# Performance work log

Hardware: AMD Instinct MI355X
Metric: run time of the kernel (lower is better)

## Reference

```python
import jax, jax.numpy as jnp
import numpy as np

jax.config.update("jax_enable_x64", True)

N = 100000   # active sparse sites
H = W = 512  # event-camera grid
CIN, CMID, COUT = 64, 384, 64
SHIFT = 16   # shift_n


def setup_inputs() -> dict:
    rng = np.random.default_rng(0)
    # unique active coordinates on the grid (batch index 0)
    flat = rng.permutation(H * W)[:N]
    ys, xs = flat // W, flat % W
    # dense index map with 1-pixel halo; sentinel N = missing neighbor
    idx_map = np.full((H + 2, W + 2), N, dtype=np.int32)
    idx_map[ys + 1, xs + 1] = np.arange(N, dtype=np.int32)
    # 3x3 neighborhood indices per active site, row-major kernel order
    nbr = np.stack([idx_map[ys + 1 + dy, xs + 1 + dx]
                    for dy in (-1, 0, 1) for dx in (-1, 0, 1)], axis=1)

    def ri(lo, hi, shape):
        return jnp.asarray(rng.integers(lo, hi, size=shape), dtype=jnp.float32)

    return {
        "feats": ri(-128, 128, (N, CIN)),      # int8-valued input features
        "w1": ri(-128, 128, (CIN, CMID)),       # 1x1 expand weights
        "b1": ri(-1024, 1024, (CMID,)),
        "s1": ri(1, 16, (CMID,)),
        "w_dw": ri(-128, 128, (9, CMID)),       # 3x3 depthwise weights [k, C]
        "b2": ri(-1024, 1024, (CMID,)),
        "s2": ri(1, 64, (CMID,)),
        "w3": ri(-128, 128, (CMID, COUT)),      # 1x1 project weights
        "b3": ri(-1024, 1024, (COUT,)),
        "s3": ri(1, 16, (COUT,)),
        "neighbor_idx": jnp.asarray(nbr),       # [N, 9] int32, N = sentinel
    }


def _quant(psum, bias, scale, relu):
    # (psum + bias) * scale, add 2^(shift-1), arithmetic >> shift,
    # clamp to int8 range, optional relu. psum values are exact integers.
    t = psum.astype(jnp.int64)
    t = ((t + bias.astype(jnp.int64)) * scale.astype(jnp.int64)
         + (1 << (SHIFT - 1))) >> SHIFT
    y = jnp.clip(t.astype(jnp.float32), -128.0, 127.0)
    return jnp.maximum(y, 0.0) if relu else y


def reference(feats, w1, b1, s1, w_dw, b2, s2, w3, b3, s3, neighbor_idx):
    # 1x1 expand (sparse 1x1 conv == matmul over active sites) + quant + relu
    x1 = _quant(feats @ w1, b1, s1, True)                       # [N, CMID]
    # 3x3 depthwise sparse conv: gather 9 neighbors (zero row for missing)
    pad = jnp.concatenate([x1, jnp.zeros((1, x1.shape[1]), x1.dtype)], axis=0)
    psum2 = jnp.einsum('nkc,kc->nc', pad[neighbor_idx], w_dw)   # [N, CMID]
    x2 = _quant(psum2, b2, s2, True)
    # 1x1 project + quant (linear bottleneck: no relu)
    x3 = _quant(x2 @ w3, b3, s3, False)                          # [N, COUT]
    return x3
```

## Files before the change

kernel.cpp:

```cpp
#include <hip/hip_runtime.h>
#include <stdint.h>

#define N_SITES 100000
#define NPAD    100032
#define CIN 64
#define CMID 384
#define COUT 64
#define SHIFT 16

typedef int   v4i __attribute__((ext_vector_type(4)));
typedef unsigned int v4u __attribute__((ext_vector_type(4)));
typedef float v4f __attribute__((ext_vector_type(4)));

__global__ __launch_bounds__(256) void pack_w(
    const float* __restrict__ w1, const float* __restrict__ w3,
    const float* __restrict__ b1, const float* __restrict__ s1,
    const float* __restrict__ b2, const float* __restrict__ s2,
    const float* __restrict__ b3, const float* __restrict__ s3,
    const float* __restrict__ wdw,
    int8_t* __restrict__ w1p, int8_t* __restrict__ w3p,
    int* __restrict__ q1, int* __restrict__ q3,
    int8_t* __restrict__ wdw8, int* __restrict__ bs2,
    int8_t* __restrict__ x1s)
{
    int o = blockIdx.x * 256 + threadIdx.x;
    if (o < 24 * 64 * 16) {
        int t = o >> 10, l = (o >> 4) & 63, b = o & 15;
        int k = ((l >> 4) << 4) + b;
        int col = t * 16 + (l & 15);
        w1p[o] = (int8_t)__float2int_rn(w1[k * CMID + col]);
    }
    int o3 = o - 24 * 64 * 16;
    if (o3 >= 0 && o3 < 6 * 4 * 64 * 16) {
        int ks = o3 >> 12, t = (o3 >> 10) & 3;
        int l = (o3 >> 4) & 63, b = o3 & 15;
        int k = ks * 64 + ((l >> 4) << 4) + b;
        int col = t * 16 + (l & 15);
        w3p[o3] = (int8_t)__float2int_rn(w3[k * COUT + col]);
    }
    if (o < 9 * CMID)
        wdw8[o] = (int8_t)__float2int_rn(wdw[o]);
    if (o < CMID) {
        q1[o] = __float2int_rn(b1[o]);
        q1[CMID + o] = __float2int_rn(s1[o]);
        int bb = __float2int_rn(b2[o]);
        int ss = __float2int_rn(s2[o]);
        bs2[o] = (bb & 0xFFFF) | (ss << 16);
        x1s[(size_t)N_SITES * CMID + o] = 0;
    }
    if (o < COUT) {
        q3[o] = __float2int_rn(b3[o]);
        q3[COUT + o] = __float2int_rn(s3[o]);
    }
}

__global__ __launch_bounds__(256) void k1_mfma(
    const float* __restrict__ feats, const int8_t* __restrict__ w1p,
    const int* __restrict__ q1, int8_t* __restrict__ x1s)
{
    __shared__ int8_t xt[64 * 400];
    const int lane = threadIdx.x & 63;
    const int wave = threadIdx.x >> 6;
    const int sl = wave * 16 + (lane & 15);
    const int site = blockIdx.x * 64 + sl;
    const int rsite = min(site, N_SITES - 1);
    const int cb = (lane >> 4) << 2;

    v4i b;
    const float* fp = feats + (size_t)rsite * CIN + ((lane >> 4) << 4);
#pragma unroll
    for (int j = 0; j < 4; ++j) {
        const v4f f = *(const v4f*)(fp + 4 * j);
        uint32_t pk = (uint32_t)(__float2int_rn(f[0]) & 255)
                    | ((uint32_t)(__float2int_rn(f[1]) & 255) << 8)
                    | ((uint32_t)(__float2int_rn(f[2]) & 255) << 16)
                    | ((uint32_t)__float2int_rn(f[3]) << 24);
        b[j] = (int)pk;
    }

    const v4i* ap = (const v4i*)w1p + lane;
#pragma unroll
    for (int t = 0; t < 24; ++t) {
        v4i a = ap[t * 64];
        v4i acc = {0, 0, 0, 0};
        acc = __builtin_amdgcn_mfma_i32_16x16x64_i8(a, b, acc, 0, 0, 0);
        const int co = t * 16 + cb;
        const v4i bi = *(const v4i*)(q1 + co);
        const v4i si = *(const v4i*)(q1 + CMID + co);
        uint32_t wrd = 0;
#pragma unroll
        for (int r = 0; r < 4; ++r) {
            int v = ((acc[r] + bi[r]) * si[r] + (1 << (SHIFT - 1))) >> SHIFT;
            v = max(0, min(127, v));
            wrd |= (uint32_t)v << (8 * r);
        }
        *(uint32_t*)(xt + sl * 400 + co) = wrd;
    }
    __syncthreads();

    int8_t* dst = x1s + (size_t)blockIdx.x * 64 * CMID;
#pragma unroll
    for (int it = 0; it < 6; ++it) {
        const int lin = it * 4096 + threadIdx.x * 16;
        const int r = lin / 384;
        const int c = lin - r * 384;
        const v4u val = *(const v4u*)(xt + r * 400 + c);
        if (blockIdx.x * 64 + r < N_SITES)
            *(v4u*)(dst + lin) = val;
    }
}

__global__ __launch_bounds__(256) void k2_dw(
    const int8_t* __restrict__ x1s, const int* __restrict__ nbr,
    const int8_t* __restrict__ wdw8, const int* __restrict__ bs2,
    int8_t* __restrict__ x2s)
{
    const int g = blockIdx.x * 256 + threadIdx.x;
    const int site = g / 24;
    const int c0 = (g - site * 24) << 4;

    const int* nb = &nbr[site * 9];
    int idx[9];
#pragma unroll
    for (int k = 0; k < 9; ++k) idx[k] = nb[k];

    v4u V[9];
#pragma unroll
    for (int k = 0; k < 9; ++k) {
        const int off = (idx[k] << 8) + (idx[k] << 7) + c0;
        V[k] = *(const v4u*)(x1s + off);
    }

    int acc[16];
#pragma unroll
    for (int j = 0; j < 16; ++j) acc[j] = 0;

#pragma unroll
    for (int k = 0; k < 9; ++k) {
        const v4u W = *(const v4u*)(wdw8 + k * CMID + c0);
#pragma unroll
        for (int j = 0; j < 4; ++j) {
#pragma unroll
            for (int b = 0; b < 4; ++b) {
                const int v = (int)(uint8_t)(V[k][j] >> (8 * b));
                const int w = (int)(int8_t)(W[j] >> (8 * b));
                acc[j * 4 + b] += v * w;
            }
        }
    }

    const v4i BS0 = *(const v4i*)(bs2 + c0);
    const v4i BS1 = *(const v4i*)(bs2 + c0 + 4);
    const v4i BS2 = *(const v4i*)(bs2 + c0 + 8);
    const v4i BS3 = *(const v4i*)(bs2 + c0 + 12);
    const v4i BS[4] = {BS0, BS1, BS2, BS3};

    v4u outw;
#pragma unroll
    for (int j = 0; j < 4; ++j) {
        uint32_t wrd = 0;
#pragma unroll
        for (int b = 0; b < 4; ++b) {
            const int bsv = BS[j][b];
            const int bb = (bsv << 16) >> 16;
            const int ss = bsv >> 16;
            int t = ((acc[j * 4 + b] + bb) * ss + (1 << (SHIFT - 1))) >> SHIFT;
            t = max(0, min(127, t));
            wrd |= (uint32_t)t << (8 * b);
        }
        outw[j] = wrd;
    }
    *(v4u*)(x2s + (site << 8) + (site << 7) + c0) = outw;
}

__global__ __launch_bounds__(256) void k3_mfma(
    const int8_t* __restrict__ x2s, const int8_t* __restrict__ w3p,
    const int* __restrict__ q3, float* __restrict__ out)
{
    __shared__ float ot[64 * 68];
    const int lane = threadIdx.x & 63;
    const int wave = threadIdx.x >> 6;
    const int sl = wave * 16 + (lane & 15);
    const int site = blockIdx.x * 64 + sl;
    const int rsite = min(site, N_SITES - 1);
    const int cb = (lane >> 4) << 2;
    const int8_t* xrow = x2s + (size_t)rsite * CMID + ((lane >> 4) << 4);

    v4i acc[4] = {{0,0,0,0},{0,0,0,0},{0,0,0,0},{0,0,0,0}};
#pragma unroll
    for (int ks = 0; ks < 6; ++ks) {
        const v4i bfr = *(const v4i*)(xrow + ks * 64);
#pragma unroll
        for (int t = 0; t < 4; ++t) {
            const v4i afr = *((const v4i*)w3p + (ks * 4 + t) * 64 + lane);
            acc[t] = __builtin_amdgcn_mfma_i32_16x16x64_i8(afr, bfr, acc[t], 0, 0, 0);
        }
    }
#pragma unroll
    for (int t = 0; t < 4; ++t) {
        const int co = t * 16 + cb;
        const v4i bo = *(const v4i*)(q3 + co);
        const v4i so = *(const v4i*)(q3 + COUT + co);
        v4f o;
#pragma unroll
        for (int r = 0; r < 4; ++r) {
            int v = ((acc[t][r] + bo[r]) * so[r] + (1 << (SHIFT - 1))) >> SHIFT;
            v = max(-128, min(127, v));
            o[r] = (float)v;
        }
        *(v4f*)(&ot[sl * 68 + co]) = o;
    }
    __syncthreads();

    float* dst = out + (size_t)blockIdx.x * 64 * COUT;
#pragma unroll
    for (int it = 0; it < 4; ++it) {
        const int lin = it * 1024 + threadIdx.x * 4;
        const int r = lin >> 6;
        const int c = lin & 63;
        const v4f val = *(const v4f*)(&ot[r * 68 + c]);
        if (blockIdx.x * 64 + r < N_SITES)
            *(v4f*)(dst + lin) = val;
    }
}

extern "C" void kernel_launch(void* const* d_in, const int* in_sizes, int n_in,
                              void* d_out, int out_size, void* d_ws, size_t ws_size,
                              hipStream_t stream) {
    const float* feats = (const float*)d_in[0];
    const float* w1    = (const float*)d_in[1];
    const float* b1    = (const float*)d_in[2];
    const float* s1    = (const float*)d_in[3];
    const float* wdw   = (const float*)d_in[4];
    const float* b2    = (const float*)d_in[5];
    const float* s2    = (const float*)d_in[6];
    const float* w3    = (const float*)d_in[7];
    const float* b3    = (const float*)d_in[8];
    const float* s3    = (const float*)d_in[9];
    const int*   nbr   = (const int*)d_in[10];
    float* out = (float*)d_out;

    int8_t* x1s   = (int8_t*)d_ws;
    int8_t* x2s   = x1s + (size_t)NPAD * CMID;
    int8_t* w1p   = x2s + (size_t)NPAD * CMID;
    int8_t* w3p   = w1p + 24 * 64 * 16;
    int*    q1    = (int*)(w3p + 6 * 4 * 64 * 16);
    int*    q3    = q1 + 2 * CMID;
    int8_t* wdw8  = (int8_t*)(q3 + 2 * COUT);
    int*    bs2   = (int*)(wdw8 + 9 * CMID);

    pack_w<<<192, 256, 0, stream>>>(w1, w3, b1, s1, b2, s2, b3, s3, wdw,
                                    w1p, w3p, q1, q3, wdw8, bs2, x1s);
    k1_mfma<<<NPAD / 64, 256, 0, stream>>>(feats, w1p, q1, x1s);
    k2_dw<<<N_SITES * 24 / 256, 256, 0, stream>>>(x1s, nbr, wdw8, bs2, x2s);
    k3_mfma<<<NPAD / 64, 256, 0, stream>>>(x2s, w3p, q3, out);
}
```

Before: 82.65 us.

## Fuse depthwise conv and projection matmul into one kernel via LDS staging

Merges the 3x3 depthwise gather kernel and the 1x1 projection MFMA kernel into a single 768-thread kernel handling 32 sites per block. The depthwise results are written to shared memory instead of a global x2 buffer, and two waves then run the MFMA projection from LDS. This removes the x2 global write and read round trip plus one launch. The cost is that 10 of 12 waves sit idle during the MFMA phase, and the large blocks may reduce occupancy.

```diff
diff --git a/kernel.cpp b/kernel.cpp
--- a/kernel.cpp
+++ b/kernel.cpp
@@ -110,117 +110,116 @@
     }
 }
 
-__global__ __launch_bounds__(256) void k2_dw(
+__global__ __launch_bounds__(768) void k23(
     const int8_t* __restrict__ x1s, const int* __restrict__ nbr,
     const int8_t* __restrict__ wdw8, const int* __restrict__ bs2,
-    int8_t* __restrict__ x2s)
+    const int8_t* __restrict__ w3p, const int* __restrict__ q3,
+    float* __restrict__ out)
 {
-    const int g = blockIdx.x * 256 + threadIdx.x;
-    const int site = g / 24;
-    const int c0 = (g - site * 24) << 4;
-
-    const int* nb = &nbr[site * 9];
-    int idx[9];
-#pragma unroll
-    for (int k = 0; k < 9; ++k) idx[k] = nb[k];
-
-    v4u V[9];
-#pragma unroll
-    for (int k = 0; k < 9; ++k) {
-        const int off = (idx[k] << 8) + (idx[k] << 7) + c0;
-        V[k] = *(const v4u*)(x1s + off);
-    }
-
-    int acc[16];
-#pragma unroll
-    for (int j = 0; j < 16; ++j) acc[j] = 0;
-
-#pragma unroll
-    for (int k = 0; k < 9; ++k) {
-        const v4u W = *(const v4u*)(wdw8 + k * CMID + c0);
+    __shared__ int8_t xt[32 * 400];
+    __shared__ float  ot[32 * 68];
+    const int tid = threadIdx.x;
+
+    {
+        const int sl = tid / 24;
+        const int c0 = (tid - sl * 24) << 4;
+        const int site = blockIdx.x * 32 + sl;
+
+        const int* nb = &nbr[site * 9];
+        int idx[9];
+#pragma unroll
+        for (int k = 0; k < 9; ++k) idx[k] = nb[k];
+
+        v4u V[9];
+#pragma unroll
+        for (int k = 0; k < 9; ++k) {
+            const int off = (idx[k] << 8) + (idx[k] << 7) + c0;
+            V[k] = *(const v4u*)(x1s + off);
+        }
+
+        int acc[16];
+#pragma unroll
+        for (int j = 0; j < 16; ++j) acc[j] = 0;
+
+#pragma unroll
+        for (int k = 0; k < 9; ++k) {
+            const v4u W = *(const v4u*)(wdw8 + k * CMID + c0);
+#pragma unroll
+            for (int j = 0; j < 4; ++j) {
+#pragma unroll
+                for (int b = 0; b < 4; ++b) {
+                    const int v = (int)(uint8_t)(V[k][j] >> (8 * b));
+                    const int w = (int)(int8_t)(W[j] >> (8 * b));
+                    acc[j * 4 + b] += v * w;
+                }
+            }
+        }
+
+        const v4i BS0 = *(const v4i*)(bs2 + c0);
+        const v4i BS1 = *(const v4i*)(bs2 + c0 + 4);
+        const v4i BS2 = *(const v4i*)(bs2 + c0 + 8);
+        const v4i BS3 = *(const v4i*)(bs2 + c0 + 12);
+        const v4i BS[4] = {BS0, BS1, BS2, BS3};
+
+        v4u outw;
 #pragma unroll
         for (int j = 0; j < 4; ++j) {
+            uint32_t wrd = 0;
 #pragma unroll
             for (int b = 0; b < 4; ++b) {
-                const int v = (int)(uint8_t)(V[k][j] >> (8 * b));
-                const int w = (int)(int8_t)(W[j] >> (8 * b));
-                acc[j * 4 + b] += v * w;
-            }
-        }
-    }
-
-    const v4i BS0 = *(const v4i*)(bs2 + c0);
-    const v4i BS1 = *(const v4i*)(bs2 + c0 + 4);
-    const v4i BS2 = *(const v4i*)(bs2 + c0 + 8);
-    const v4i BS3 = *(const v4i*)(bs2 + c0 + 12);
-    const v4i BS[4] = {BS0, BS1, BS2, BS3};
-
-    v4u outw;
-#pragma unroll
-    for (int j = 0; j < 4; ++j) {
-        uint32_t wrd = 0;
-#pragma unroll
-        for (int b = 0; b < 4; ++b) {
-            const int bsv = BS[j][b];
-            const int bb = (bsv << 16) >> 16;
-            const int ss = bsv >> 16;
-            int t = ((acc[j * 4 + b] + bb) * ss + (1 << (SHIFT - 1))) >> SHIFT;
-            t = max(0, min(127, t));
-            wrd |= (uint32_t)t << (8 * b);
-        }
-        outw[j] = wrd;
-    }
-    *(v4u*)(x2s + (site << 8) + (site << 7) + c0) = outw;
-}
-
-__global__ __launch_bounds__(256) void k3_mfma(
-    const int8_t* __restrict__ x2s, const int8_t* __restrict__ w3p,
-    const int* __restrict__ q3, float* __restrict__ out)
-{
-    __shared__ float ot[64 * 68];
-    const int lane = threadIdx.x & 63;
-    const int wave = threadIdx.x >> 6;
-    const int sl = wave * 16 + (lane & 15);
-    const int site = blockIdx.x * 64 + sl;
-    const int rsite = min(site, N_SITES - 1);
-    const int cb = (lane >> 4) << 2;
-    const int8_t* xrow = x2s + (size_t)rsite * CMID + ((lane >> 4) << 4);
-
-    v4i acc[4] = {{0,0,0,0},{0,0,0,0},{0,0,0,0},{0,0,0,0}};
-#pragma unroll
-    for (int ks = 0; ks < 6; ++ks) {
-        const v4i bfr = *(const v4i*)(xrow + ks * 64);
+                const int bsv = BS[j][b];
+                const int bb = (bsv << 16) >> 16;
+                const int ss = bsv >> 16;
+                int t = ((acc[j * 4 + b] + bb) * ss + (1 << (SHIFT - 1))) >> SHIFT;
+                t = max(0, min(127, t));
+                wrd |= (uint32_t)t << (8 * b);
+            }
+            outw[j] = wrd;
+        }
+        *(v4u*)(xt + sl * 400 + c0) = outw;
+    }
+    __syncthreads();
+
+    const int wv = tid >> 6;
+    if (wv < 2) {
+        const int lane = tid & 63;
+        const int sl2 = wv * 16 + (lane & 15);
+        const int cb = (lane >> 4) << 2;
+        const int8_t* xrow = xt + sl2 * 400 + ((lane >> 4) << 4);
+
+        v4i acc[4] = {{0,0,0,0},{0,0,0,0},{0,0,0,0},{0,0,0,0}};
+#pragma unroll
+        for (int ks = 0; ks < 6; ++ks) {
+            const v4i bfr = *(const v4i*)(xrow + ks * 64);
+#pragma unroll
+            for (int t = 0; t < 4; ++t) {
+                const v4i afr = *((const v4i*)w3p + (ks * 4 + t) * 64 + lane);
+                acc[t] = __builtin_amdgcn_mfma_i32_16x16x64_i8(afr, bfr, acc[t], 0, 0, 0);
+            }
+        }
 #pragma unroll
         for (int t = 0; t < 4; ++t) {
-            const v4i afr = *((const v4i*)w3p + (ks * 4 + t) * 64 + lane);
-            acc[t] = __builtin_amdgcn_mfma_i32_16x16x64_i8(afr, bfr, acc[t], 0, 0, 0);
-        }
-    }
-#pragma unroll
-    for (int t = 0; t < 4; ++t) {
-        const int co = t * 16 + cb;
-        const v4i bo = *(const v4i*)(q3 + co);
-        const v4i so = *(const v4i*)(q3 + COUT + co);
-        v4f o;
-#pragma unroll
-        for (int r = 0; r < 4; ++r) {
-            int v = ((acc[t][r] + bo[r]) * so[r] + (1 << (SHIFT - 1))) >> SHIFT;
-            v = max(-128, min(127, v));
-            o[r] = (float)v;
-        }
-        *(v4f*)(&ot[sl * 68 + co]) = o;
+            const int co = t * 16 + cb;
+            const v4i bo = *(const v4i*)(q3 + co);
+            const v4i so = *(const v4i*)(q3 + COUT + co);
+            v4f o;
+#pragma unroll
+            for (int r = 0; r < 4; ++r) {
+                int v = ((acc[t][r] + bo[r]) * so[r] + (1 << (SHIFT - 1))) >> SHIFT;
+                v = max(-128, min(127, v));
+                o[r] = (float)v;
+            }
+            *(v4f*)(&ot[sl2 * 68 + co]) = o;
+        }
     }
     __syncthreads();
 
-    float* dst = out + (size_t)blockIdx.x * 64 * COUT;
-#pragma unroll
-    for (int it = 0; it < 4; ++it) {
-        const int lin = it * 1024 + threadIdx.x * 4;
+    if (tid < 512) {
+        const int lin = tid * 4;
         const int r = lin >> 6;
         const int c = lin & 63;
         const v4f val = *(const v4f*)(&ot[r * 68 + c]);
-        if (blockIdx.x * 64 + r < N_SITES)
-            *(v4f*)(dst + lin) = val;
+        *(v4f*)(out + (size_t)blockIdx.x * 32 * COUT + lin) = val;
     }
 }
 
@@ -241,8 +240,7 @@
     float* out = (float*)d_out;
 
     int8_t* x1s   = (int8_t*)d_ws;
-    int8_t* x2s   = x1s + (size_t)NPAD * CMID;
-    int8_t* w1p   = x2s + (size_t)NPAD * CMID;
+    int8_t* w1p   = x1s + (size_t)(NPAD + 64) * CMID;
     int8_t* w3p   = w1p + 24 * 64 * 16;
     int*    q1    = (int*)(w3p + 6 * 4 * 64 * 16);
     int*    q3    = q1 + 2 * CMID;
@@ -252,6 +250,5 @@
     pack_w<<<192, 256, 0, stream>>>(w1, w3, b1, s1, b2, s2, b3, s3, wdw,
                                     w1p, w3p, q1, q3, wdw8, bs2, x1s);
     k1_mfma<<<NPAD / 64, 256, 0, stream>>>(feats, w1p, q1, x1s);
-    k2_dw<<<N_SITES * 24 / 256, 256, 0, stream>>>(x1s, nbr, wdw8, bs2, x2s);
-    k3_mfma<<<NPAD / 64, 256, 0, stream>>>(x2s, w3p, q3, out);
-}
+    k23<<<N_SITES / 32, 768, 0, stream>>>(x1s, nbr, wdw8, bs2, w3p, q3, out);
+}
```

New measurement: 91.01 us. +10.1%, slower.

## Compute depthwise 3x3 conv with i8 MFMA using diagonal-packed weights

Applied to the files above, without the earlier changes.

The scalar per-thread depthwise kernel is replaced by a kernel that treats each 16-channel group as an MFMA 16x16x64 i8 product. The weight matrix is packed so each 16-wide tap block is diagonal, which lets the gathered neighbor rows act as the B operand. Outputs are staged in LDS and written back as coalesced rows. The MFMA path does 16x redundant multiplies on zero weights and changes the gather pattern, aiming to offload the int multiply-accumulate work from the VALU.

```diff
diff --git a/kernel.cpp b/kernel.cpp
--- a/kernel.cpp
+++ b/kernel.cpp
@@ -19,8 +19,8 @@
     const float* __restrict__ b3, const float* __restrict__ s3,
     const float* __restrict__ wdw,
     int8_t* __restrict__ w1p, int8_t* __restrict__ w3p,
-    int* __restrict__ q1, int* __restrict__ q3,
-    int8_t* __restrict__ wdw8, int* __restrict__ bs2,
+    int8_t* __restrict__ w2t,
+    int* __restrict__ q1, int* __restrict__ q3, int* __restrict__ bs2,
     int8_t* __restrict__ x1s)
 {
     int o = blockIdx.x * 256 + threadIdx.x;
@@ -38,8 +38,20 @@
         int col = t * 16 + (l & 15);
         w3p[o3] = (int8_t)__float2int_rn(w3[k * COUT + col]);
     }
-    if (o < 9 * CMID)
-        wdw8[o] = (int8_t)__float2int_rn(wdw[o]);
+    int o4 = o - 48 * 64 * 16;
+    if (o4 >= 0 && o4 < 24 * 3 * 64 * 16) {
+        int cg = o4 / 3072;
+        int rem = o4 - cg * 3072;
+        int kk = rem >> 10;
+        int l  = (rem >> 4) & 63;
+        int b  = o4 & 15;
+        int q  = l >> 4;
+        int tap = kk * 4 + q;
+        int8_t val = 0;
+        if (tap < 9 && b == (l & 15))
+            val = (int8_t)__float2int_rn(wdw[tap * CMID + cg * 16 + b]);
+        w2t[o4] = val;
+    }
     if (o < CMID) {
         q1[o] = __float2int_rn(b1[o]);
         q1[CMID + o] = __float2int_rn(s1[o]);
@@ -110,67 +122,64 @@
     }
 }
 
-__global__ __launch_bounds__(256) void k2_dw(
+__global__ __launch_bounds__(128) void k2_mfma(
     const int8_t* __restrict__ x1s, const int* __restrict__ nbr,
-    const int8_t* __restrict__ wdw8, const int* __restrict__ bs2,
+    const int8_t* __restrict__ w2t, const int* __restrict__ bs2,
     int8_t* __restrict__ x2s)
 {
-    const int g = blockIdx.x * 256 + threadIdx.x;
-    const int site = g / 24;
-    const int c0 = (g - site * 24) << 4;
-
-    const int* nb = &nbr[site * 9];
-    int idx[9];
-#pragma unroll
-    for (int k = 0; k < 9; ++k) idx[k] = nb[k];
-
-    v4u V[9];
-#pragma unroll
-    for (int k = 0; k < 9; ++k) {
-        const int off = (idx[k] << 8) + (idx[k] << 7) + c0;
-        V[k] = *(const v4u*)(x1s + off);
-    }
-
-    int acc[16];
-#pragma unroll
-    for (int j = 0; j < 16; ++j) acc[j] = 0;
-
-#pragma unroll
-    for (int k = 0; k < 9; ++k) {
-        const v4u W = *(const v4u*)(wdw8 + k * CMID + c0);
-#pragma unroll
-        for (int j = 0; j < 4; ++j) {
-#pragma unroll
-            for (int b = 0; b < 4; ++b) {
-                const int v = (int)(uint8_t)(V[k][j] >> (8 * b));
-                const int w = (int)(int8_t)(W[j] >> (8 * b));
-                acc[j * 4 + b] += v * w;
-            }
-        }
-    }
-
-    const v4i BS0 = *(const v4i*)(bs2 + c0);
-    const v4i BS1 = *(const v4i*)(bs2 + c0 + 4);
-    const v4i BS2 = *(const v4i*)(bs2 + c0 + 8);
-    const v4i BS3 = *(const v4i*)(bs2 + c0 + 12);
-    const v4i BS[4] = {BS0, BS1, BS2, BS3};
-
-    v4u outw;
-#pragma unroll
-    for (int j = 0; j < 4; ++j) {
+    __shared__ int8_t xt[2][16 * 400];
+    const int lane = threadIdx.x & 63;
+    const int wv = threadIdx.x >> 6;
+    const int site0 = (blockIdx.x * 2 + wv) * 16;
+    int8_t* xw = &xt[wv][0];
+    const int q  = lane >> 4;
+    const int sl = lane & 15;
+    const int site = site0 + sl;
+
+    int off[3];
+#pragma unroll
+    for (int kk = 0; kk < 3; ++kk) {
+        int tap = kk * 4 + q;
+        if (tap > 8) tap = 8;
+        const int idx = nbr[site * 9 + tap];
+        off[kk] = (idx << 8) + (idx << 7);
+    }
+
+#pragma unroll 1
+    for (int cg = 0; cg < 24; ++cg) {
+        const int c0 = cg << 4;
+        v4i acc = {0, 0, 0, 0};
+#pragma unroll
+        for (int kk = 0; kk < 3; ++kk) {
+            const v4i bfr = *(const v4i*)(x1s + off[kk] + c0);
+            const v4i afr = *((const v4i*)w2t + (cg * 3 + kk) * 64 + lane);
+            acc = __builtin_amdgcn_mfma_i32_16x16x64_i8(afr, bfr, acc, 0, 0, 0);
+        }
+        const v4i bsv = *(const v4i*)(bs2 + c0 + (q << 2));
         uint32_t wrd = 0;
 #pragma unroll
-        for (int b = 0; b < 4; ++b) {
-            const int bsv = BS[j][b];
-            const int bb = (bsv << 16) >> 16;
-            const int ss = bsv >> 16;
-            int t = ((acc[j * 4 + b] + bb) * ss + (1 << (SHIFT - 1))) >> SHIFT;
+        for (int r = 0; r < 4; ++r) {
+            const int bb = (bsv[r] << 16) >> 16;
+            const int ss = bsv[r] >> 16;
+            int t = ((acc[r] + bb) * ss + (1 << (SHIFT - 1))) >> SHIFT;
             t = max(0, min(127, t));
-            wrd |= (uint32_t)t << (8 * b);
-        }
-        outw[j] = wrd;
-    }
-    *(v4u*)(x2s + (site << 8) + (site << 7) + c0) = outw;
+            wrd |= (uint32_t)t << (8 * r);
+        }
+        *(uint32_t*)(xw + sl * 400 + c0 + (q << 2)) = wrd;
+    }
+
+    __builtin_amdgcn_wave_barrier();
+    asm volatile("s_waitcnt lgkmcnt(0)" ::: "memory");
+    __builtin_amdgcn_wave_barrier();
+
+    int8_t* dst = x2s + (size_t)site0 * CMID;
+#pragma unroll
+    for (int it = 0; it < 6; ++it) {
+        const int lin = it * 1024 + lane * 16;
+        const int r = lin / 384;
+        const int c = lin - r * 384;
+        *(v4u*)(dst + lin) = *(const v4u*)(xw + r * 400 + c);
+    }
 }
 
 __global__ __launch_bounds__(256) void k3_mfma(
@@ -240,18 +249,18 @@
     const int*   nbr   = (const int*)d_in[10];
     float* out = (float*)d_out;
 
-    int8_t* x1s   = (int8_t*)d_ws;
-    int8_t* x2s   = x1s + (size_t)NPAD * CMID;
-    int8_t* w1p   = x2s + (size_t)NPAD * CMID;
-    int8_t* w3p   = w1p + 24 * 64 * 16;
-    int*    q1    = (int*)(w3p + 6 * 4 * 64 * 16);
-    int*    q3    = q1 + 2 * CMID;
-    int8_t* wdw8  = (int8_t*)(q3 + 2 * COUT);
-    int*    bs2   = (int*)(wdw8 + 9 * CMID);
-
-    pack_w<<<192, 256, 0, stream>>>(w1, w3, b1, s1, b2, s2, b3, s3, wdw,
-                                    w1p, w3p, q1, q3, wdw8, bs2, x1s);
+    int8_t* x1s  = (int8_t*)d_ws;
+    int8_t* x2s  = x1s + (size_t)(NPAD + 64) * CMID;
+    int8_t* w1p  = x2s + (size_t)NPAD * CMID;
+    int8_t* w3p  = w1p + 24 * 64 * 16;
+    int*    q1   = (int*)(w3p + 6 * 4 * 64 * 16);
+    int*    q3   = q1 + 2 * CMID;
+    int8_t* w2t  = (int8_t*)(q3 + 2 * COUT);
+    int*    bs2  = (int*)(w2t + 24 * 3 * 64 * 16);
+
+    pack_w<<<480, 256, 0, stream>>>(w1, w3, b1, s1, b2, s2, b3, s3, wdw,
+                                    w1p, w3p, w2t, q1, q3, bs2, x1s);
     k1_mfma<<<NPAD / 64, 256, 0, stream>>>(feats, w1p, q1, x1s);
-    k2_dw<<<N_SITES * 24 / 256, 256, 0, stream>>>(x1s, nbr, wdw8, bs2, x2s);
+    k2_mfma<<<N_SITES / 32, 128, 0, stream>>>(x1s, nbr, w2t, bs2, x2s);
     k3_mfma<<<NPAD / 64, 256, 0, stream>>>(x2s, w3p, q3, out);
 }
```

Result: slower. 119.1 us (+44.1%).

## Remap depthwise kernel so each wave shares a channel chunk across 64 sites

Applied to the files above, without the earlier changes.

The depthwise conv kernel now assigns one 16-channel chunk per wave, with each lane handling a different site. The channel index is wave-uniform via readfirstlane, so depthwise weights, bias and scale can be fetched as scalar loads; they are stored as int32 and the multiplies use mul24. Output goes through shared memory so x2 rows are written as coalesced 64-byte segments. The trade-off is that a lane's nine gathered 16-byte neighbour loads are now spread across different sites rather than contiguous channels, and neighbour indices are re-read six times per site.

```diff
diff --git a/kernel.cpp b/kernel.cpp
--- a/kernel.cpp
+++ b/kernel.cpp
@@ -20,7 +20,7 @@
     const float* __restrict__ wdw,
     int8_t* __restrict__ w1p, int8_t* __restrict__ w3p,
     int* __restrict__ q1, int* __restrict__ q3,
-    int8_t* __restrict__ wdw8, int* __restrict__ bs2,
+    int* __restrict__ wdw32, int* __restrict__ q2b, int* __restrict__ q2s,
     int8_t* __restrict__ x1s)
 {
     int o = blockIdx.x * 256 + threadIdx.x;
@@ -39,13 +39,12 @@
         w3p[o3] = (int8_t)__float2int_rn(w3[k * COUT + col]);
     }
     if (o < 9 * CMID)
-        wdw8[o] = (int8_t)__float2int_rn(wdw[o]);
+        wdw32[o] = __float2int_rn(wdw[o]);
     if (o < CMID) {
         q1[o] = __float2int_rn(b1[o]);
         q1[CMID + o] = __float2int_rn(s1[o]);
-        int bb = __float2int_rn(b2[o]);
-        int ss = __float2int_rn(s2[o]);
-        bs2[o] = (bb & 0xFFFF) | (ss << 16);
+        q2b[o] = __float2int_rn(b2[o]);
+        q2s[o] = __float2int_rn(s2[o]);
         x1s[(size_t)N_SITES * CMID + o] = 0;
     }
     if (o < COUT) {
@@ -112,65 +111,68 @@
 
 __global__ __launch_bounds__(256) void k2_dw(
     const int8_t* __restrict__ x1s, const int* __restrict__ nbr,
-    const int8_t* __restrict__ wdw8, const int* __restrict__ bs2,
-    int8_t* __restrict__ x2s)
-{
-    const int g = blockIdx.x * 256 + threadIdx.x;
-    const int site = g / 24;
-    const int c0 = (g - site * 24) << 4;
-
-    const int* nb = &nbr[site * 9];
+    const int* __restrict__ wdw32, const int* __restrict__ q2b,
+    const int* __restrict__ q2s, int8_t* __restrict__ x2s)
+{
+    __shared__ int8_t xw[64][68];
+    const int lane = threadIdx.x & 63;
+    const int wv = threadIdx.x >> 6;
+    const int sg = blockIdx.x / 6;
+    const int cq = blockIdx.x - sg * 6;
+    const int chunk = __builtin_amdgcn_readfirstlane(cq * 4 + wv);
+    const int c0 = chunk << 4;
+    const int site = sg * 64 + lane;
+    const int rsite = min(site, N_SITES - 1);
+
+    const int* nb = nbr + rsite * 9;
     int idx[9];
 #pragma unroll
     for (int k = 0; k < 9; ++k) idx[k] = nb[k];
 
     v4u V[9];
 #pragma unroll
+    for (int k = 0; k < 9; ++k)
+        V[k] = *(const v4u*)(x1s + (size_t)idx[k] * CMID + c0);
+
+    int acc[16];
+#pragma unroll
+    for (int j = 0; j < 16; ++j) acc[j] = 0;
+
+#pragma unroll
     for (int k = 0; k < 9; ++k) {
-        const int off = (idx[k] << 8) + (idx[k] << 7) + c0;
-        V[k] = *(const v4u*)(x1s + off);
-    }
-
-    int acc[16];
-#pragma unroll
-    for (int j = 0; j < 16; ++j) acc[j] = 0;
-
-#pragma unroll
-    for (int k = 0; k < 9; ++k) {
-        const v4u W = *(const v4u*)(wdw8 + k * CMID + c0);
+        const int* wr = wdw32 + k * CMID + c0;
 #pragma unroll
         for (int j = 0; j < 4; ++j) {
 #pragma unroll
             for (int b = 0; b < 4; ++b) {
-                const int v = (int)(uint8_t)(V[k][j] >> (8 * b));
-                const int w = (int)(int8_t)(W[j] >> (8 * b));
-                acc[j * 4 + b] += v * w;
+                const int v = (int)((V[k][j] >> (8 * b)) & 0xff);
+                acc[j * 4 + b] = __mul24(v, wr[j * 4 + b]) + acc[j * 4 + b];
             }
         }
     }
 
-    const v4i BS0 = *(const v4i*)(bs2 + c0);
-    const v4i BS1 = *(const v4i*)(bs2 + c0 + 4);
-    const v4i BS2 = *(const v4i*)(bs2 + c0 + 8);
-    const v4i BS3 = *(const v4i*)(bs2 + c0 + 12);
-    const v4i BS[4] = {BS0, BS1, BS2, BS3};
-
-    v4u outw;
+    const int* bbp = q2b + c0;
+    const int* ssp = q2s + c0;
 #pragma unroll
     for (int j = 0; j < 4; ++j) {
         uint32_t wrd = 0;
 #pragma unroll
         for (int b = 0; b < 4; ++b) {
-            const int bsv = BS[j][b];
-            const int bb = (bsv << 16) >> 16;
-            const int ss = bsv >> 16;
-            int t = ((acc[j * 4 + b] + bb) * ss + (1 << (SHIFT - 1))) >> SHIFT;
+            const int c = j * 4 + b;
+            int t = (__mul24(acc[c] + bbp[c], ssp[c]) + (1 << (SHIFT - 1))) >> SHIFT;
             t = max(0, min(127, t));
             wrd |= (uint32_t)t << (8 * b);
         }
-        outw[j] = wrd;
-    }
-    *(v4u*)(x2s + (site << 8) + (site << 7) + c0) = outw;
+        *(uint32_t*)(&xw[lane][wv * 16 + j * 4]) = wrd;
+    }
+    __syncthreads();
+
+    const int sr = threadIdx.x >> 2;
+    const int sq = threadIdx.x & 3;
+    if (sg * 64 + sr < N_SITES) {
+        const v4u val = *(const v4u*)(&xw[sr][sq * 16]);
+        *(v4u*)(x2s + (size_t)(sg * 64 + sr) * CMID + cq * 64 + sq * 16) = val;
+    }
 }
 
 __global__ __launch_bounds__(256) void k3_mfma(
@@ -246,12 +248,13 @@
     int8_t* w3p   = w1p + 24 * 64 * 16;
     int*    q1    = (int*)(w3p + 6 * 4 * 64 * 16);
     int*    q3    = q1 + 2 * CMID;
-    int8_t* wdw8  = (int8_t*)(q3 + 2 * COUT);
-    int*    bs2   = (int*)(wdw8 + 9 * CMID);
+    int*    wdw32 = q3 + 2 * COUT;
+    int*    q2b   = wdw32 + 9 * CMID;
+    int*    q2s   = q2b + CMID;
 
     pack_w<<<192, 256, 0, stream>>>(w1, w3, b1, s1, b2, s2, b3, s3, wdw,
-                                    w1p, w3p, q1, q3, wdw8, bs2, x1s);
+                                    w1p, w3p, q1, q3, wdw32, q2b, q2s, x1s);
     k1_mfma<<<NPAD / 64, 256, 0, stream>>>(feats, w1p, q1, x1s);
-    k2_dw<<<N_SITES * 24 / 256, 256, 0, stream>>>(x1s, nbr, wdw8, bs2, x2s);
+    k2_dw<<<1563 * 6, 256, 0, stream>>>(x1s, nbr, wdw32, q2b, q2s, x2s);
     k3_mfma<<<NPAD / 64, 256, 0, stream>>>(x2s, w3p, q3, out);
 }
```

After: 101.4 us. +22.6%, slower.
